# Performance work log

Measured on AMD Instinct MI355X. Metric: run time of the kernel, lower is better.

The kernel has to match this reference:

```python
import jax, jax.numpy as jnp
import numpy as np

N_NODES = 50000
N_EDGES = 800000
D_IN = 128
D_OUT = 128
N_GRAPHS = 512
N_CONVS = 5
EPS = 1e-5


def setup_inputs() -> dict:
    key = jax.random.key(0)
    ks = jax.random.split(key, 8)
    x = jax.random.normal(ks[0], (N_NODES, D_IN), dtype=jnp.float32)
    edge_index = jax.random.randint(ks[1], (2, N_EDGES), 0, N_NODES, dtype=jnp.int32)
    batch = jnp.sort(jax.random.randint(ks[2], (N_NODES,), 0, N_GRAPHS, dtype=jnp.int32))
    s = 1.0 / np.sqrt(D_IN)
    W_rel = jax.random.normal(ks[3], (N_CONVS, D_OUT, D_IN), dtype=jnp.float32) * s
    b_rel = jax.random.normal(ks[4], (N_CONVS, D_OUT), dtype=jnp.float32) * s
    W_root = jax.random.normal(ks[5], (N_CONVS, D_OUT, D_IN), dtype=jnp.float32) * s
    gamma = jnp.ones((D_OUT,), dtype=jnp.float32)
    beta = jnp.zeros((D_OUT,), dtype=jnp.float32)
    Wc = jax.random.normal(ks[6], (96, D_OUT), dtype=jnp.float32) * (1.0 / np.sqrt(D_OUT))
    bc = jax.random.normal(ks[7], (96,), dtype=jnp.float32) * (1.0 / np.sqrt(D_OUT))
    return {"x": x, "edge_index": edge_index, "batch": batch, "i": 0,
            "W_rel": W_rel, "b_rel": b_rel, "W_root": W_root,
            "gamma": gamma, "beta": beta, "Wc": Wc, "bc": bc}


def reference(x, edge_index, batch, i, W_rel, b_rel, W_root, gamma, beta, Wc, bc):
    # --- 5 GraphConv branches, summed. GraphConv: lin_rel(sum_{j->i} x_j) + lin_root(x).
    # Sum over the 5 convs commutes with the linears, so fold the weights first.
    src, dst = edge_index[0], edge_index[1]
    agg = jax.ops.segment_sum(x[src], dst, num_segments=N_NODES)  # [N, D_in]
    Wr = jnp.sum(W_rel, axis=0)   # [D_out, D_in]
    Wt = jnp.sum(W_root, axis=0)  # [D_out, D_in]
    br = jnp.sum(b_rel, axis=0)   # [D_out]
    h = agg @ Wr.T + x @ Wt.T + br  # [N, D_out]
    # --- NodeLevelBatchNorm (training: batch stats over all nodes, biased var)
    mean = jnp.mean(h, axis=0)
    var = jnp.mean((h - mean) ** 2, axis=0)
    h = gamma * (h - mean) * jax.lax.rsqrt(var + EPS) + beta
    # --- global max pool over graphs, relu, classifier (i=0 -> no-dropout branch)
    pooled = jax.ops.segment_max(h, batch, num_segments=N_GRAPHS)  # [G, D_out]
    pooled = jax.nn.relu(pooled)
    return pooled @ Wc.T + bc  # [G, 96]
```

## Files before the change

kernel.cpp:

```cpp
#include <hip/hip_runtime.h>

#define EPS 1e-5f

constexpr int NN = 50000, NE = 800000, DD = 128, NG = 512, NC = 5, NO = 96;
constexpr int MAXB = 8192;
constexpr int NBUCK = 196;

typedef __attribute__((ext_vector_type(8))) short bf16x8;
typedef __attribute__((ext_vector_type(4))) float f32x4;

constexpr size_t HB   = 0;
constexpr size_t XB   = (size_t)NN * DD / 2;
constexpr size_t WB   = XB + (size_t)NN * DD / 2;
constexpr size_t BRO  = WB + DD * 256 / 2;
constexpr size_t CSUM = BRO + DD;
constexpr size_t CSQ  = CSUM + 4 * DD;
constexpr size_t POOL = CSQ + 4 * DD;
constexpr size_t ZLEN = 8 * DD + (size_t)NG * DD;
constexpr size_t GCNT = POOL + (size_t)NG * DD;
constexpr size_t ROFF = GCNT + 256;
constexpr size_t BSTOR= ROFF + NN + 1;
constexpr size_t CSR16= BSTOR + (size_t)NBUCK*MAXB;

constexpr int XCAST_B = NN * DD / 4 / 256;
constexpr int FOLD_B  = DD * DD / 256;
constexpr int BUCK_B  = (NE + 4095) / 4096;

static __device__ __forceinline__ unsigned short f2b(float f) {
    unsigned int u = __float_as_uint(f);
    return (unsigned short)((u + 0x7FFFu + ((u >> 16) & 1u)) >> 16);
}
static __device__ __forceinline__ float b2f(unsigned short h) {
    return __uint_as_float(((unsigned int)h) << 16);
}
static __device__ __forceinline__ unsigned fkey(float f) {
    unsigned u = __float_as_uint(f);
    return (u >> 31) ? ~u : (u | 0x80000000u);
}
static __device__ __forceinline__ float unfkey(unsigned k) {
    unsigned u = (k & 0x80000000u) ? (k ^ 0x80000000u) : ~k;
    return __uint_as_float(u);
}

__global__ __launch_bounds__(256) void k_prep(const float* __restrict__ x,
                                              const float* __restrict__ Wrel,
                                              const float* __restrict__ brel,
                                              const float* __restrict__ Wroot,
                                              const int* __restrict__ ei,
                                              float* __restrict__ ws, int* __restrict__ wi) {
    __shared__ int lcnt[256];
    __shared__ int lbase[256];
    int b = blockIdx.x, t = threadIdx.x;
    if (b < XCAST_B) {
        int i = b * 256 + t;
        float4 v = ((const float4*)x)[i];
        ushort4 o = {f2b(v.x), f2b(v.y), f2b(v.z), f2b(v.w)};
        ((ushort4*)(ws + XB))[i] = o;
    } else if (b < XCAST_B + FOLD_B) {
        int idx = (b - XCAST_B) * 256 + t;
        int k = idx >> 7, o = idx & 127;
        float wr = 0.f, wt = 0.f;
        for (int c = 0; c < NC; ++c) {
            wr += Wrel [c*DD*DD + o*DD + k];
            wt += Wroot[c*DD*DD + o*DD + k];
        }
        unsigned short* wb = (unsigned short*)(ws + WB);
        wb[o*256 + k]       = f2b(wr);
        wb[o*256 + 128 + k] = f2b(wt);
        if (k == 0) {
            float bias = 0.f;
            for (int c = 0; c < NC; ++c) bias += brel[c*DD + o];
            ws[BRO + o] = bias;
        }
    } else {
        int bb = b - XCAST_B - FOLD_B;
        lcnt[t] = 0;
        __syncthreads();
        int val[16], krk[16];
        #pragma unroll
        for (int j = 0; j < 16; ++j) {
            int e = bb * 4096 + j * 256 + t;
            krk[j] = -1;
            if (e < NE) {
                int d = ei[NE + e], s = ei[e];
                int key = d >> 8;
                int r = atomicAdd(&lcnt[key], 1);
                val[j] = s | ((d & 255) << 16);
                krk[j] = (key << 16) | r;
            }
        }
        __syncthreads();
        if (t < NBUCK && lcnt[t] > 0)
            lbase[t] = atomicAdd(&wi[GCNT + t], lcnt[t]);
        __syncthreads();
        #pragma unroll
        for (int j = 0; j < 16; ++j) {
            if (krk[j] >= 0) {
                int key = krk[j] >> 16, r = krk[j] & 0xFFFF;
                int p = lbase[key] + r;
                if (p < MAXB) wi[BSTOR + (size_t)key * MAXB + p] = val[j];
            }
        }
    }
}

__global__ __launch_bounds__(256) void k_sort(int* __restrict__ wi) {
    __shared__ int eds[MAXB];
    __shared__ unsigned short srt[MAXB];
    __shared__ int cnt[256], cnt2[256], lscan[256], gall[256];
    int t = threadIdx.x, b = blockIdx.x;
    for (size_t i = (size_t)b * 256 + t; i < ZLEN; i += (size_t)NBUCK * 256)
        wi[CSUM + i] = 0;
    int g = wi[GCNT + t];
    gall[t] = g; lscan[t] = g; cnt[t] = 0;
    __syncthreads();
    for (int off = 1; off < 256; off <<= 1) {
        int u = (t >= off) ? gall[t - off] : 0;
        __syncthreads();
        gall[t] += u;
        __syncthreads();
    }
    int base = gall[b] - lscan[b];
    int C = lscan[b]; if (C > MAXB) C = MAXB;
    __syncthreads();
    for (int i = t; i < C; i += 256) {
        int v = wi[BSTOR + (size_t)b * MAXB + i];
        eds[i] = v;
        atomicAdd(&cnt[v >> 16], 1);
    }
    __syncthreads();
    int cv = cnt[t];
    for (int off = 1; off < 256; off <<= 1) {
        int u = (t >= off) ? cnt[t - off] : 0;
        __syncthreads();
        cnt[t] += u;
        __syncthreads();
    }
    lscan[t] = cnt[t] - cv;
    cnt2[t] = 0;
    __syncthreads();
    int n = b * 256 + t;
    if (n < NN) wi[ROFF + n] = base + lscan[t];
    if (b == 0 && t == 0) wi[ROFF + NN] = NE;
    for (int i = t; i < C; i += 256) {
        int v = eds[i], k = v >> 16;
        int p = lscan[k] + atomicAdd(&cnt2[k], 1);
        srt[p] = (unsigned short)(v & 0xFFFF);
    }
    __syncthreads();
    unsigned short* csr = (unsigned short*)(wi + CSR16);
    for (int i = t; i < C; i += 256)
        csr[base + i] = srt[i];
}

__global__ __launch_bounds__(256) void k_gather(const int* __restrict__ wi,
                                                float* __restrict__ ws) {
    const unsigned short* xb = (const unsigned short*)(ws + XB);
    const unsigned short* csr = (const unsigned short*)(wi + CSR16);
    unsigned short* hb = (unsigned short*)(ws + HB);
    int tid = threadIdx.x;
    int n   = blockIdx.x * 16 + (tid >> 4);
    int sub = tid & 15;
    int c8  = sub * 8;
    if (n >= NN) return;
    int e0 = wi[ROFF + n], e1 = wi[ROFF + n + 1];
    int cnt = e1 - e0;
    float acc0[8] = {}, acc1[8] = {};
    int base = 0;
    for (; base + 16 <= cnt; base += 16) {
        int myE = (int)csr[e0 + base + sub];
        #pragma unroll
        for (int h = 0; h < 2; ++h) {
            bf16x8 v[8];
            #pragma unroll
            for (int j = 0; j < 8; ++j) {
                int s = __shfl(myE, h * 8 + j, 16);
                v[j] = *(const bf16x8*)&xb[(size_t)s * DD + c8];
            }
            #pragma unroll
            for (int j = 0; j < 8; ++j)
                #pragma unroll
                for (int c = 0; c < 8; ++c)
                    ((j & 1) ? acc1 : acc0)[c] += b2f((unsigned short)v[j][c]);
        }
    }
    int rem = cnt - base;
    if (rem > 0) {
        int myE = (sub < rem) ? (int)csr[e0 + base + sub] : 0;
        int j = 0;
        for (; j + 8 <= rem; j += 8) {
            bf16x8 v[8];
            #pragma unroll
            for (int q = 0; q < 8; ++q) {
                int s = __shfl(myE, j + q, 16);
                v[q] = *(const bf16x8*)&xb[(size_t)s * DD + c8];
            }
            #pragma unroll
            for (int q = 0; q < 8; ++q)
                #pragma unroll
                for (int c = 0; c < 8; ++c)
                    ((q & 1) ? acc1 : acc0)[c] += b2f((unsigned short)v[q][c]);
        }
        if (j + 4 <= rem) {
            bf16x8 v[4];
            #pragma unroll
            for (int q = 0; q < 4; ++q) {
                int s = __shfl(myE, j + q, 16);
                v[q] = *(const bf16x8*)&xb[(size_t)s * DD + c8];
            }
            #pragma unroll
            for (int q = 0; q < 4; ++q)
                #pragma unroll
                for (int c = 0; c < 8; ++c)
                    ((q & 1) ? acc1 : acc0)[c] += b2f((unsigned short)v[q][c]);
            j += 4;
        }
        for (; j < rem; ++j) {
            int s = __shfl(myE, j, 16);
            bf16x8 v = *(const bf16x8*)&xb[(size_t)s * DD + c8];
            #pragma unroll
            for (int c = 0; c < 8; ++c) acc0[c] += b2f((unsigned short)v[c]);
        }
    }
    bf16x8 o;
    #pragma unroll
    for (int c = 0; c < 8; ++c) o[c] = (short)f2b(acc0[c] + acc1[c]);
    *(bf16x8*)&hb[(size_t)n * DD + c8] = o;
}

__global__ __launch_bounds__(256) void k_gemm(const int* __restrict__ batch,
                                              float* __restrict__ ws) {
    __shared__ float sSum[128], sSq[128];
    __shared__ int batchS[64];
    __shared__ unsigned maxS[8][128];
    const unsigned short* hb = (const unsigned short*)(ws + HB);
    const unsigned short* xb = (const unsigned short*)(ws + XB);
    const unsigned short* wb = (const unsigned short*)(ws + WB);
    unsigned* poolU = (unsigned*)(ws + POOL);
    int tid  = threadIdx.x;
    if (tid < 128) { sSum[tid] = 0.f; sSq[tid] = 0.f; }
    for (int i = tid; i < 8 * 128; i += 256) ((unsigned*)maxS)[i] = 0u;
    if (tid < 64) {
        int r = blockIdx.x * 64 + tid; if (r > NN - 1) r = NN - 1;
        batchS[tid] = batch[r];
    }
    __syncthreads();
    int gBase = batchS[0];
    int wave = tid >> 6, lane = tid & 63;
    int quad = lane >> 4, l16 = lane & 15;
    int cw = wave * 32;
    bf16x8 bf[2][8];
    #pragma unroll
    for (int nt = 0; nt < 2; ++nt)
        #pragma unroll
        for (int kt = 0; kt < 8; ++kt)
            bf[nt][kt] = *(const bf16x8*)(wb + (size_t)(cw + nt*16 + l16)*256 + kt*32 + quad*8);
    float bias[2] = { ws[BRO + cw + l16], ws[BRO + cw + 16 + l16] };
    float csum[2] = {}, csq[2] = {};
    #pragma unroll
    for (int rt = 0; rt < 4; ++rt) {
        int lbase = rt * 16;
        int row0 = blockIdx.x * 64 + lbase;
        int arow = row0 + l16; if (arow > NN - 1) arow = NN - 1;
        const unsigned short* aggRow = hb + (size_t)arow * DD;
        const unsigned short* xRow   = xb + (size_t)arow * DD;
        bf16x8 af[8];
        #pragma unroll
        for (int kt = 0; kt < 8; ++kt)
            af[kt] = *(const bf16x8*)((kt < 4 ? aggRow + kt*32 : xRow + kt*32 - 128) + quad*8);
        f32x4 acc[2] = {};
        #pragma unroll
        for (int kt = 0; kt < 8; ++kt)
            #pragma unroll
            for (int nt = 0; nt < 2; ++nt)
                acc[nt] = __builtin_amdgcn_mfma_f32_16x16x32_bf16(af[kt], bf[nt][kt], acc[nt], 0, 0, 0);
        #pragma unroll
        for (int nt = 0; nt < 2; ++nt) {
            int col = cw + nt*16 + l16;
            float mx = 0.f; int gcur = -1;
            #pragma unroll
            for (int r = 0; r < 4; ++r) {
                int row = row0 + quad*4 + r;
                if (row < NN) {
                    float v = acc[nt][r] + bias[nt];
                    csum[nt] += v; csq[nt] += v * v;
                    int g = batchS[lbase + quad*4 + r];
                    if (g != gcur) {
                        if (gcur >= 0) {
                            int rel = gcur - gBase;
                            if (rel < 8) atomicMax(&maxS[rel][col], fkey(mx));
                            else atomicMax(&poolU[(size_t)gcur * DD + col], fkey(mx));
                        }
                        gcur = g; mx = v;
                    } else mx = fmaxf(mx, v);
                }
            }
            if (gcur >= 0) {
                int rel = gcur - gBase;
                if (rel < 8) atomicMax(&maxS[rel][col], fkey(mx));
                else atomicMax(&poolU[(size_t)gcur * DD + col], fkey(mx));
            }
        }
    }
    __syncthreads();
    int span = batchS[63] - gBase + 1; if (span > 8) span = 8;
    for (int i = tid; i < span * 128; i += 256) {
        unsigned k = maxS[i >> 7][i & 127];
        if (k) atomicMax(&poolU[(size_t)(gBase + (i >> 7)) * DD + (i & 127)], k);
    }
    #pragma unroll
    for (int nt = 0; nt < 2; ++nt) {
        int col = cw + nt*16 + l16;
        float cs = csum[nt], cq = csq[nt];
        cs += __shfl_xor(cs, 16); cs += __shfl_xor(cs, 32);
        cq += __shfl_xor(cq, 16); cq += __shfl_xor(cq, 32);
        if (quad == 0) { atomicAdd(&sSum[col], cs); atomicAdd(&sSq[col], cq); }
    }
    __syncthreads();
    if (tid < 128) {
        int slot = (blockIdx.x & 3) * DD;
        atomicAdd(&ws[CSUM + slot + tid], sSum[tid]);
        atomicAdd(&ws[CSQ  + slot + tid], sSq[tid]);
    }
}

__global__ __launch_bounds__(128) void k_out(const float* __restrict__ gamma,
                                             const float* __restrict__ beta,
                                             const float* __restrict__ Wc,
                                             const float* __restrict__ bc,
                                             const float* __restrict__ ws,
                                             float* __restrict__ out) {
    __shared__ float pS[128];
    int g = blockIdx.x, t = threadIdx.x;
    float s = ws[CSUM + t] + ws[CSUM + DD + t] + ws[CSUM + 2*DD + t] + ws[CSUM + 3*DD + t];
    float q = ws[CSQ  + t] + ws[CSQ  + DD + t] + ws[CSQ  + 2*DD + t] + ws[CSQ  + 3*DD + t];
    float mean = s * (1.0f / NN);
    float var  = q * (1.0f / NN) - mean * mean;
    float sc   = gamma[t] * rsqrtf(var + EPS);
    float sh   = beta[t] - sc * mean;
    unsigned k = ((const unsigned*)(ws + POOL))[(size_t)g * DD + t];
    float p = 0.f;
    if (k) p = fmaxf(unfkey(k) * sc + sh, 0.f);
    pS[t] = p;
    __syncthreads();
    if (t < NO) {
        float acc = bc[t];
        #pragma unroll 8
        for (int kk = 0; kk < DD; ++kk) acc += pS[kk] * Wc[t*DD + kk];
        out[g*NO + t] = acc;
    }
}

extern "C" void kernel_launch(void* const* d_in, const int* in_sizes, int n_in,
                              void* d_out, int out_size, void* d_ws, size_t ws_size,
                              hipStream_t stream) {
    const float* x     = (const float*)d_in[0];
    const int*   ei    = (const int*)  d_in[1];
    const int*   batch = (const int*)  d_in[2];
    const float* Wrel  = (const float*)d_in[4];
    const float* brel  = (const float*)d_in[5];
    const float* Wroot = (const float*)d_in[6];
    const float* gamma = (const float*)d_in[7];
    const float* beta  = (const float*)d_in[8];
    const float* Wc    = (const float*)d_in[9];
    const float* bc    = (const float*)d_in[10];
    float* ws  = (float*)d_ws;
    int*   wi  = (int*)d_ws;
    float* out = (float*)d_out;

    hipMemsetAsync(wi + GCNT, 0, 256 * sizeof(int), stream);

    k_prep  <<<XCAST_B + FOLD_B + BUCK_B, 256, 0, stream>>>(x, Wrel, brel, Wroot, ei, ws, wi);
    k_sort  <<<NBUCK, 256, 0, stream>>>(wi);
    k_gather<<<(NN + 15)/16, 256, 0, stream>>>(wi, ws);
    k_gemm  <<<(NN + 63)/64, 256, 0, stream>>>(batch, ws);
    k_out   <<<NG, 128, 0, stream>>>(gamma, beta, Wc, bc, ws, out);
}
```

Baseline: 183.5 us.

## Fuse all stages into one persistent kernel with software grid barriers

Replaces the five separate kernel launches with a single persistent kernel of 512 blocks. The blocks loop over virtual block indices for each phase (prep, bucket sort, gather, GEMM+pool, output) and separate the phases with atomic-counter grid barriers. The memset of the bucket counters moves into the kernel's zeroing phase. This removes per-launch overhead and tail gaps between kernels. In exchange it relies on all 512 blocks being co-resident to avoid deadlock, adds spin-wait barrier cost, and limits parallelism per phase to the fixed grid size.

```diff
diff --git a/kernel.cpp b/kernel.cpp
--- a/kernel.cpp
+++ b/kernel.cpp
@@ -5,6 +5,7 @@
 constexpr int NN = 50000, NE = 800000, DD = 128, NG = 512, NC = 5, NO = 96;
 constexpr int MAXB = 8192;
 constexpr int NBUCK = 196;
+constexpr int GRIDB = 512;
 
 typedef __attribute__((ext_vector_type(8))) short bf16x8;
 typedef __attribute__((ext_vector_type(4))) float f32x4;
@@ -16,15 +17,19 @@
 constexpr size_t CSUM = BRO + DD;
 constexpr size_t CSQ  = CSUM + 4 * DD;
 constexpr size_t POOL = CSQ + 4 * DD;
-constexpr size_t ZLEN = 8 * DD + (size_t)NG * DD;
 constexpr size_t GCNT = POOL + (size_t)NG * DD;
-constexpr size_t ROFF = GCNT + 256;
+constexpr size_t ZLEN = 8 * DD + (size_t)NG * DD + 256;
+constexpr size_t BAR  = GCNT + 256;
+constexpr size_t ROFF = BAR + 8;
 constexpr size_t BSTOR= ROFF + NN + 1;
 constexpr size_t CSR16= BSTOR + (size_t)NBUCK*MAXB;
 
 constexpr int XCAST_B = NN * DD / 4 / 256;
 constexpr int FOLD_B  = DD * DD / 256;
 constexpr int BUCK_B  = (NE + 4095) / 4096;
+constexpr int PREP_V  = XCAST_B + FOLD_B + BUCK_B;
+constexpr int GATH_V  = (NN + 15) / 16;
+constexpr int GEMM_V  = (NN + 63) / 64;
 
 static __device__ __forceinline__ unsigned short f2b(float f) {
     unsigned int u = __float_as_uint(f);
@@ -42,312 +47,353 @@
     return __uint_as_float(u);
 }
 
-__global__ __launch_bounds__(256) void k_prep(const float* __restrict__ x,
-                                              const float* __restrict__ Wrel,
-                                              const float* __restrict__ brel,
-                                              const float* __restrict__ Wroot,
-                                              const int* __restrict__ ei,
-                                              float* __restrict__ ws, int* __restrict__ wi) {
-    __shared__ int lcnt[256];
-    __shared__ int lbase[256];
-    int b = blockIdx.x, t = threadIdx.x;
-    if (b < XCAST_B) {
-        int i = b * 256 + t;
-        float4 v = ((const float4*)x)[i];
-        ushort4 o = {f2b(v.x), f2b(v.y), f2b(v.z), f2b(v.w)};
-        ((ushort4*)(ws + XB))[i] = o;
-    } else if (b < XCAST_B + FOLD_B) {
-        int idx = (b - XCAST_B) * 256 + t;
-        int k = idx >> 7, o = idx & 127;
-        float wr = 0.f, wt = 0.f;
-        for (int c = 0; c < NC; ++c) {
-            wr += Wrel [c*DD*DD + o*DD + k];
-            wt += Wroot[c*DD*DD + o*DD + k];
+static __device__ __forceinline__ void gridbar(int* bar, int idx, int nb) {
+    __syncthreads();
+    if (threadIdx.x == 0) {
+        __threadfence();
+        atomicAdd(&bar[idx], 1);
+        while (atomicAdd(&bar[idx], 0) < nb)
+            __builtin_amdgcn_s_sleep(8);
+        __threadfence();
+    }
+    __syncthreads();
+}
+
+__global__ __launch_bounds__(256, 2) void k_mega(const float* __restrict__ x,
+                                                 const float* __restrict__ Wrel,
+                                                 const float* __restrict__ brel,
+                                                 const float* __restrict__ Wroot,
+                                                 const int* __restrict__ ei,
+                                                 const int* __restrict__ batch,
+                                                 const float* __restrict__ gamma,
+                                                 const float* __restrict__ beta,
+                                                 const float* __restrict__ Wc,
+                                                 const float* __restrict__ bc,
+                                                 float* __restrict__ ws,
+                                                 int* __restrict__ wi,
+                                                 float* __restrict__ out) {
+    __shared__ __align__(16) char smem[53248];
+    const int t   = threadIdx.x;
+    const int bid = blockIdx.x;
+    const int nb  = gridDim.x;
+    int* bar = wi + BAR;
+
+    for (size_t i = (size_t)bid * 256 + t; i < ZLEN; i += (size_t)nb * 256)
+        wi[CSUM + i] = 0;
+    gridbar(bar, 0, nb);
+
+    {
+        int* lcnt  = (int*)(smem + 49152);
+        int* lbase = (int*)(smem + 50176);
+        for (int vb = bid; vb < PREP_V; vb += nb) {
+            if (vb < XCAST_B) {
+                int i = vb * 256 + t;
+                float4 v = ((const float4*)x)[i];
+                ushort4 o = {f2b(v.x), f2b(v.y), f2b(v.z), f2b(v.w)};
+                ((ushort4*)(ws + XB))[i] = o;
+            } else if (vb < XCAST_B + FOLD_B) {
+                int idx = (vb - XCAST_B) * 256 + t;
+                int k = idx >> 7, o = idx & 127;
+                float wr = 0.f, wt = 0.f;
+                for (int c = 0; c < NC; ++c) {
+                    wr += Wrel [c*DD*DD + o*DD + k];
+                    wt += Wroot[c*DD*DD + o*DD + k];
+                }
+                unsigned short* wb = (unsigned short*)(ws + WB);
+                wb[o*256 + k]       = f2b(wr);
+                wb[o*256 + 128 + k] = f2b(wt);
+                if (k == 0) {
+                    float bias = 0.f;
+                    for (int c = 0; c < NC; ++c) bias += brel[c*DD + o];
+                    ws[BRO + o] = bias;
+                }
+            } else {
+                int bb = vb - XCAST_B - FOLD_B;
+                lcnt[t] = 0;
+                __syncthreads();
+                int val[16], krk[16];
+                #pragma unroll
+                for (int j = 0; j < 16; ++j) {
+                    int e = bb * 4096 + j * 256 + t;
+                    krk[j] = -1;
+                    if (e < NE) {
+                        int d = ei[NE + e], s = ei[e];
+                        int key = d >> 8;
+                        int r = atomicAdd(&lcnt[key], 1);
+                        val[j] = s | ((d & 255) << 16);
+                        krk[j] = (key << 16) | r;
+                    }
+                }
+                __syncthreads();
+                if (t < NBUCK && lcnt[t] > 0)
+                    lbase[t] = atomicAdd(&wi[GCNT + t], lcnt[t]);
+                __syncthreads();
+                #pragma unroll
+                for (int j = 0; j < 16; ++j) {
+                    if (krk[j] >= 0) {
+                        int key = krk[j] >> 16, r = krk[j] & 0xFFFF;
+                        int p = lbase[key] + r;
+                        if (p < MAXB) wi[BSTOR + (size_t)key * MAXB + p] = val[j];
+                    }
+                }
+                __syncthreads();
+            }
         }
-        unsigned short* wb = (unsigned short*)(ws + WB);
-        wb[o*256 + k]       = f2b(wr);
-        wb[o*256 + 128 + k] = f2b(wt);
-        if (k == 0) {
-            float bias = 0.f;
-            for (int c = 0; c < NC; ++c) bias += brel[c*DD + o];
-            ws[BRO + o] = bias;
+    }
+    gridbar(bar, 1, nb);
+
+    {
+        int* eds   = (int*)smem;
+        unsigned short* srt = (unsigned short*)(smem + 32768);
+        int* cnt   = (int*)(smem + 49152);
+        int* cnt2  = (int*)(smem + 50176);
+        int* lscan = (int*)(smem + 51200);
+        int* gall  = (int*)(smem + 52224);
+        for (int b = bid; b < NBUCK; b += nb) {
+            int g = wi[GCNT + t];
+            gall[t] = g; lscan[t] = g; cnt[t] = 0;
+            __syncthreads();
+            for (int off = 1; off < 256; off <<= 1) {
+                int u = (t >= off) ? gall[t - off] : 0;
+                __syncthreads();
+                gall[t] += u;
+                __syncthreads();
+            }
+            int base = gall[b] - lscan[b];
+            int C = lscan[b]; if (C > MAXB) C = MAXB;
+            __syncthreads();
+            for (int i = t; i < C; i += 256) {
+                int v = wi[BSTOR + (size_t)b * MAXB + i];
+                eds[i] = v;
+                atomicAdd(&cnt[v >> 16], 1);
+            }
+            __syncthreads();
+            int cv = cnt[t];
+            for (int off = 1; off < 256; off <<= 1) {
+                int u = (t >= off) ? cnt[t - off] : 0;
+                __syncthreads();
+                cnt[t] += u;
+                __syncthreads();
+            }
+            lscan[t] = cnt[t] - cv;
+            cnt2[t] = 0;
+            __syncthreads();
+            int n = b * 256 + t;
+            if (n < NN) wi[ROFF + n] = base + lscan[t];
+            if (b == 0 && t == 0) wi[ROFF + NN] = NE;
+            for (int i = t; i < C; i += 256) {
+                int v = eds[i], k = v >> 16;
+                int p = lscan[k] + atomicAdd(&cnt2[k], 1);
+                srt[p] = (unsigned short)(v & 0xFFFF);
+            }
+            __syncthreads();
+            unsigned short* csr = (unsigned short*)(wi + CSR16);
+            for (int i = t; i < C; i += 256)
+                csr[base + i] = srt[i];
         }
-    } else {
-        int bb = b - XCAST_B - FOLD_B;
-        lcnt[t] = 0;
-        __syncthreads();
-        int val[16], krk[16];
-        #pragma unroll
-        for (int j = 0; j < 16; ++j) {
-            int e = bb * 4096 + j * 256 + t;
-            krk[j] = -1;
-            if (e < NE) {
-                int d = ei[NE + e], s = ei[e];
-                int key = d >> 8;
-                int r = atomicAdd(&lcnt[key], 1);
-                val[j] = s | ((d & 255) << 16);
-                krk[j] = (key << 16) | r;
+    }
+    gridbar(bar, 2, nb);
+
+    {
+        const unsigned short* xb  = (const unsigned short*)(ws + XB);
+        const unsigned short* csr = (const unsigned short*)(wi + CSR16);
+        unsigned short* hb = (unsigned short*)(ws + HB);
+        int sub = t & 15;
+        int c8  = sub * 8;
+        for (int vb = bid; vb < GATH_V; vb += nb) {
+            int n = vb * 16 + (t >> 4);
+            if (n < NN) {
+                int e0 = wi[ROFF + n], e1 = wi[ROFF + n + 1];
+                int cnt = e1 - e0;
+                float acc0[8] = {}, acc1[8] = {};
+                int base = 0;
+                for (; base + 16 <= cnt; base += 16) {
+                    int myE = (int)csr[e0 + base + sub];
+                    #pragma unroll
+                    for (int h = 0; h < 2; ++h) {
+                        bf16x8 v[8];
+                        #pragma unroll
+                        for (int j = 0; j < 8; ++j) {
+                            int s = __shfl(myE, h * 8 + j, 16);
+                            v[j] = *(const bf16x8*)&xb[(size_t)s * DD + c8];
+                        }
+                        #pragma unroll
+                        for (int j = 0; j < 8; ++j)
+                            #pragma unroll
+                            for (int c = 0; c < 8; ++c)
+                                ((j & 1) ? acc1 : acc0)[c] += b2f((unsigned short)v[j][c]);
+                    }
+                }
+                int rem = cnt - base;
+                if (rem > 0) {
+                    int myE = (sub < rem) ? (int)csr[e0 + base + sub] : 0;
+                    int j = 0;
+                    for (; j + 8 <= rem; j += 8) {
+                        bf16x8 v[8];
+                        #pragma unroll
+                        for (int q = 0; q < 8; ++q) {
+                            int s = __shfl(myE, j + q, 16);
+                            v[q] = *(const bf16x8*)&xb[(size_t)s * DD + c8];
+                        }
+                        #pragma unroll
+                        for (int q = 0; q < 8; ++q)
+                            #pragma unroll
+                            for (int c = 0; c < 8; ++c)
+                                ((q & 1) ? acc1 : acc0)[c] += b2f((unsigned short)v[q][c]);
+                    }
+                    if (j + 4 <= rem) {
+                        bf16x8 v[4];
+                        #pragma unroll
+                        for (int q = 0; q < 4; ++q) {
+                            int s = __shfl(myE, j + q, 16);
+                            v[q] = *(const bf16x8*)&xb[(size_t)s * DD + c8];
+                        }
+                        #pragma unroll
+                        for (int q = 0; q < 4; ++q)
+                            #pragma unroll
+                            for (int c = 0; c < 8; ++c)
+                                ((q & 1) ? acc1 : acc0)[c] += b2f((unsigned short)v[q][c]);
+                        j += 4;
+                    }
+                    for (; j < rem; ++j) {
+                        int s = __shfl(myE, j, 16);
+                        bf16x8 v = *(const bf16x8*)&xb[(size_t)s * DD + c8];
+                        #pragma unroll
+                        for (int c = 0; c < 8; ++c) acc0[c] += b2f((unsigned short)v[c]);
+                    }
+                }
+                bf16x8 o;
+                #pragma unroll
+                for (int c = 0; c < 8; ++c) o[c] = (short)f2b(acc0[c] + acc1[c]);
+                *(bf16x8*)&hb[(size_t)n * DD + c8] = o;
             }
         }
-        __syncthreads();
-        if (t < NBUCK && lcnt[t] > 0)
-            lbase[t] = atomicAdd(&wi[GCNT + t], lcnt[t]);
-        __syncthreads();
-        #pragma unroll
-        for (int j = 0; j < 16; ++j) {
-            if (krk[j] >= 0) {
-                int key = krk[j] >> 16, r = krk[j] & 0xFFFF;
-                int p = lbase[key] + r;
-                if (p < MAXB) wi[BSTOR + (size_t)key * MAXB + p] = val[j];
-            }
-        }
-    }
-}
-
-__global__ __launch_bounds__(256) void k_sort(int* __restrict__ wi) {
-    __shared__ int eds[MAXB];
-    __shared__ unsigned short srt[MAXB];
-    __shared__ int cnt[256], cnt2[256], lscan[256], gall[256];
-    int t = threadIdx.x, b = blockIdx.x;
-    for (size_t i = (size_t)b * 256 + t; i < ZLEN; i += (size_t)NBUCK * 256)
-        wi[CSUM + i] = 0;
-    int g = wi[GCNT + t];
-    gall[t] = g; lscan[t] = g; cnt[t] = 0;
-    __syncthreads();
-    for (int off = 1; off < 256; off <<= 1) {
-        int u = (t >= off) ? gall[t - off] : 0;
-        __syncthreads();
-        gall[t] += u;
-        __syncthreads();
-    }
-    int base = gall[b] - lscan[b];
-    int C = lscan[b]; if (C > MAXB) C = MAXB;
-    __syncthreads();
-    for (int i = t; i < C; i += 256) {
-        int v = wi[BSTOR + (size_t)b * MAXB + i];
-        eds[i] = v;
-        atomicAdd(&cnt[v >> 16], 1);
-    }
-    __syncthreads();
-    int cv = cnt[t];
-    for (int off = 1; off < 256; off <<= 1) {
-        int u = (t >= off) ? cnt[t - off] : 0;
-        __syncthreads();
-        cnt[t] += u;
-        __syncthreads();
-    }
-    lscan[t] = cnt[t] - cv;
-    cnt2[t] = 0;
-    __syncthreads();
-    int n = b * 256 + t;
-    if (n < NN) wi[ROFF + n] = base + lscan[t];
-    if (b == 0 && t == 0) wi[ROFF + NN] = NE;
-    for (int i = t; i < C; i += 256) {
-        int v = eds[i], k = v >> 16;
-        int p = lscan[k] + atomicAdd(&cnt2[k], 1);
-        srt[p] = (unsigned short)(v & 0xFFFF);
-    }
-    __syncthreads();
-    unsigned short* csr = (unsigned short*)(wi + CSR16);
-    for (int i = t; i < C; i += 256)
-        csr[base + i] = srt[i];
-}
-
-__global__ __launch_bounds__(256) void k_gather(const int* __restrict__ wi,
-                                                float* __restrict__ ws) {
-    const unsigned short* xb = (const unsigned short*)(ws + XB);
-    const unsigned short* csr = (const unsigned short*)(wi + CSR16);
-    unsigned short* hb = (unsigned short*)(ws + HB);
-    int tid = threadIdx.x;
-    int n   = blockIdx.x * 16 + (tid >> 4);
-    int sub = tid & 15;
-    int c8  = sub * 8;
-    if (n >= NN) return;
-    int e0 = wi[ROFF + n], e1 = wi[ROFF + n + 1];
-    int cnt = e1 - e0;
-    float acc0[8] = {}, acc1[8] = {};
-    int base = 0;
-    for (; base + 16 <= cnt; base += 16) {
-        int myE = (int)csr[e0 + base + sub];
-        #pragma unroll
-        for (int h = 0; h < 2; ++h) {
-            bf16x8 v[8];
-            #pragma unroll
-            for (int j = 0; j < 8; ++j) {
-                int s = __shfl(myE, h * 8 + j, 16);
-                v[j] = *(const bf16x8*)&xb[(size_t)s * DD + c8];
-            }
-            #pragma unroll
-            for (int j = 0; j < 8; ++j)
-                #pragma unroll
-                for (int c = 0; c < 8; ++c)
-                    ((j & 1) ? acc1 : acc0)[c] += b2f((unsigned short)v[j][c]);
-        }
-    }
-    int rem = cnt - base;
-    if (rem > 0) {
-        int myE = (sub < rem) ? (int)csr[e0 + base + sub] : 0;
-        int j = 0;
-        for (; j + 8 <= rem; j += 8) {
-            bf16x8 v[8];
-            #pragma unroll
-            for (int q = 0; q < 8; ++q) {
-                int s = __shfl(myE, j + q, 16);
-                v[q] = *(const bf16x8*)&xb[(size_t)s * DD + c8];
-            }
-            #pragma unroll
-            for (int q = 0; q < 8; ++q)
-                #pragma unroll
-                for (int c = 0; c < 8; ++c)
-                    ((q & 1) ? acc1 : acc0)[c] += b2f((unsigned short)v[q][c]);
-        }
-        if (j + 4 <= rem) {
-            bf16x8 v[4];
-            #pragma unroll
-            for (int q = 0; q < 4; ++q) {
-                int s = __shfl(myE, j + q, 16);
-                v[q] = *(const bf16x8*)&xb[(size_t)s * DD + c8];
-            }
-            #pragma unroll
-            for (int q = 0; q < 4; ++q)
-                #pragma unroll
-                for (int c = 0; c < 8; ++c)
-                    ((q & 1) ? acc1 : acc0)[c] += b2f((unsigned short)v[q][c]);
-            j += 4;
-        }
-        for (; j < rem; ++j) {
-            int s = __shfl(myE, j, 16);
-            bf16x8 v = *(const bf16x8*)&xb[(size_t)s * DD + c8];
-            #pragma unroll
-            for (int c = 0; c < 8; ++c) acc0[c] += b2f((unsigned short)v[c]);
-        }
-    }
-    bf16x8 o;
-    #pragma unroll
-    for (int c = 0; c < 8; ++c) o[c] = (short)f2b(acc0[c] + acc1[c]);
-    *(bf16x8*)&hb[(size_t)n * DD + c8] = o;
-}
-
-__global__ __launch_bounds__(256) void k_gemm(const int* __restrict__ batch,
-                                              float* __restrict__ ws) {
-    __shared__ float sSum[128], sSq[128];
-    __shared__ int batchS[64];
-    __shared__ unsigned maxS[8][128];
-    const unsigned short* hb = (const unsigned short*)(ws + HB);
-    const unsigned short* xb = (const unsigned short*)(ws + XB);
-    const unsigned short* wb = (const unsigned short*)(ws + WB);
-    unsigned* poolU = (unsigned*)(ws + POOL);
-    int tid  = threadIdx.x;
-    if (tid < 128) { sSum[tid] = 0.f; sSq[tid] = 0.f; }
-    for (int i = tid; i < 8 * 128; i += 256) ((unsigned*)maxS)[i] = 0u;
-    if (tid < 64) {
-        int r = blockIdx.x * 64 + tid; if (r > NN - 1) r = NN - 1;
-        batchS[tid] = batch[r];
-    }
-    __syncthreads();
-    int gBase = batchS[0];
-    int wave = tid >> 6, lane = tid & 63;
-    int quad = lane >> 4, l16 = lane & 15;
-    int cw = wave * 32;
-    bf16x8 bf[2][8];
-    #pragma unroll
-    for (int nt = 0; nt < 2; ++nt)
-        #pragma unroll
-        for (int kt = 0; kt < 8; ++kt)
-            bf[nt][kt] = *(const bf16x8*)(wb + (size_t)(cw + nt*16 + l16)*256 + kt*32 + quad*8);
-    float bias[2] = { ws[BRO + cw + l16], ws[BRO + cw + 16 + l16] };
-    float csum[2] = {}, csq[2] = {};
-    #pragma unroll
-    for (int rt = 0; rt < 4; ++rt) {
-        int lbase = rt * 16;
-        int row0 = blockIdx.x * 64 + lbase;
-        int arow = row0 + l16; if (arow > NN - 1) arow = NN - 1;
-        const unsigned short* aggRow = hb + (size_t)arow * DD;
-        const unsigned short* xRow   = xb + (size_t)arow * DD;
-        bf16x8 af[8];
-        #pragma unroll
-        for (int kt = 0; kt < 8; ++kt)
-            af[kt] = *(const bf16x8*)((kt < 4 ? aggRow + kt*32 : xRow + kt*32 - 128) + quad*8);
-        f32x4 acc[2] = {};
-        #pragma unroll
-        for (int kt = 0; kt < 8; ++kt)
+    }
+    gridbar(bar, 3, nb);
+
+    {
+        float* sSum = (float*)smem;
+        float* sSq  = (float*)(smem + 512);
+        int*   batchS = (int*)(smem + 1024);
+        unsigned (*maxS)[128] = (unsigned(*)[128])(smem + 1536);
+        const unsigned short* hb = (const unsigned short*)(ws + HB);
+        const unsigned short* xb = (const unsigned short*)(ws + XB);
+        const unsigned short* wb = (const unsigned short*)(ws + WB);
+        unsigned* poolU = (unsigned*)(ws + POOL);
+        int wave = t >> 6, lane = t & 63;
+        int quad = lane >> 4, l16 = lane & 15;
+        int cw = wave * 32;
+        for (int vb = bid; vb < GEMM_V; vb += nb) {
+            if (t < 128) { sSum[t] = 0.f; sSq[t] = 0.f; }
+            for (int i = t; i < 8 * 128; i += 256) ((unsigned*)maxS)[i] = 0u;
+            if (t < 64) {
+                int r = vb * 64 + t; if (r > NN - 1) r = NN - 1;
+                batchS[t] = batch[r];
+            }
+            __syncthreads();
+            int gBase = batchS[0];
+            bf16x8 bf[2][8];
             #pragma unroll
             for (int nt = 0; nt < 2; ++nt)
-                acc[nt] = __builtin_amdgcn_mfma_f32_16x16x32_bf16(af[kt], bf[nt][kt], acc[nt], 0, 0, 0);
-        #pragma unroll
-        for (int nt = 0; nt < 2; ++nt) {
-            int col = cw + nt*16 + l16;
-            float mx = 0.f; int gcur = -1;
+                #pragma unroll
+                for (int kt = 0; kt < 8; ++kt)
+                    bf[nt][kt] = *(const bf16x8*)(wb + (size_t)(cw + nt*16 + l16)*256 + kt*32 + quad*8);
+            float bias[2] = { ws[BRO + cw + l16], ws[BRO + cw + 16 + l16] };
+            float csum[2] = {}, csq[2] = {};
             #pragma unroll
-            for (int r = 0; r < 4; ++r) {
-                int row = row0 + quad*4 + r;
-                if (row < NN) {
-                    float v = acc[nt][r] + bias[nt];
-                    csum[nt] += v; csq[nt] += v * v;
-                    int g = batchS[lbase + quad*4 + r];
-                    if (g != gcur) {
-                        if (gcur >= 0) {
-                            int rel = gcur - gBase;
-                            if (rel < 8) atomicMax(&maxS[rel][col], fkey(mx));
-                            else atomicMax(&poolU[(size_t)gcur * DD + col], fkey(mx));
+            for (int rt = 0; rt < 4; ++rt) {
+                int lbase = rt * 16;
+                int row0 = vb * 64 + lbase;
+                int arow = row0 + l16; if (arow > NN - 1) arow = NN - 1;
+                const unsigned short* aggRow = hb + (size_t)arow * DD;
+                const unsigned short* xRow   = xb + (size_t)arow * DD;
+                bf16x8 af[8];
+                #pragma unroll
+                for (int kt = 0; kt < 8; ++kt)
+                    af[kt] = *(const bf16x8*)((kt < 4 ? aggRow + kt*32 : xRow + kt*32 - 128) + quad*8);
+                f32x4 acc[2] = {};
+                #pragma unroll
+                for (int kt = 0; kt < 8; ++kt)
+                    #pragma unroll
+                    for (int nt = 0; nt < 2; ++nt)
+                        acc[nt] = __builtin_amdgcn_mfma_f32_16x16x32_bf16(af[kt], bf[nt][kt], acc[nt], 0, 0, 0);
+                #pragma unroll
+                for (int nt = 0; nt < 2; ++nt) {
+                    int col = cw + nt*16 + l16;
+                    float mx = 0.f; int gcur = -1;
+                    #pragma unroll
+                    for (int r = 0; r < 4; ++r) {
+                        int row = row0 + quad*4 + r;
+                        if (row < NN) {
+                            float v = acc[nt][r] + bias[nt];
+                            csum[nt] += v; csq[nt] += v * v;
+                            int g = batchS[lbase + quad*4 + r];
+                            if (g != gcur) {
+                                if (gcur >= 0) {
+                                    int rel = gcur - gBase;
+                                    if (rel < 8) atomicMax(&maxS[rel][col], fkey(mx));
+                                    else atomicMax(&poolU[(size_t)gcur * DD + col], fkey(mx));
+                                }
+                                gcur = g; mx = v;
+                            } else mx = fmaxf(mx, v);
                         }
-                        gcur = g; mx = v;
-                    } else mx = fmaxf(mx, v);
-                }
-            }
-            if (gcur >= 0) {
-                int rel = gcur - gBase;
-                if (rel < 8) atomicMax(&maxS[rel][col], fkey(mx));
-                else atomicMax(&poolU[(size_t)gcur * DD + col], fkey(mx));
-            }
+                    }
+                    if (gcur >= 0) {
+                        int rel = gcur - gBase;
+                        if (rel < 8) atomicMax(&maxS[rel][col], fkey(mx));
+                        else atomicMax(&poolU[(size_t)gcur * DD + col], fkey(mx));
+                    }
+                }
+            }
+            __syncthreads();
+            int span = batchS[63] - gBase + 1; if (span > 8) span = 8;
+            for (int i = t; i < span * 128; i += 256) {
+                unsigned k = maxS[i >> 7][i & 127];
+                if (k) atomicMax(&poolU[(size_t)(gBase + (i >> 7)) * DD + (i & 127)], k);
+            }
+            #pragma unroll
+            for (int nt = 0; nt < 2; ++nt) {
+                int col = cw + nt*16 + l16;
+                float cs = csum[nt], cq = csq[nt];
+                cs += __shfl_xor(cs, 16); cs += __shfl_xor(cs, 32);
+                cq += __shfl_xor(cq, 16); cq += __shfl_xor(cq, 32);
+                if (quad == 0) { atomicAdd(&sSum[col], cs); atomicAdd(&sSq[col], cq); }
+            }
+            __syncthreads();
+            if (t < 128) {
+                int slot = (vb & 3) * DD;
+                atomicAdd(&ws[CSUM + slot + t], sSum[t]);
+                atomicAdd(&ws[CSQ  + slot + t], sSq[t]);
+            }
+            __syncthreads();
         }
     }
-    __syncthreads();
-    int span = batchS[63] - gBase + 1; if (span > 8) span = 8;
-    for (int i = tid; i < span * 128; i += 256) {
-        unsigned k = maxS[i >> 7][i & 127];
-        if (k) atomicMax(&poolU[(size_t)(gBase + (i >> 7)) * DD + (i & 127)], k);
-    }
-    #pragma unroll
-    for (int nt = 0; nt < 2; ++nt) {
-        int col = cw + nt*16 + l16;
-        float cs = csum[nt], cq = csq[nt];
-        cs += __shfl_xor(cs, 16); cs += __shfl_xor(cs, 32);
-        cq += __shfl_xor(cq, 16); cq += __shfl_xor(cq, 32);
-        if (quad == 0) { atomicAdd(&sSum[col], cs); atomicAdd(&sSq[col], cq); }
-    }
-    __syncthreads();
-    if (tid < 128) {
-        int slot = (blockIdx.x & 3) * DD;
-        atomicAdd(&ws[CSUM + slot + tid], sSum[tid]);
-        atomicAdd(&ws[CSQ  + slot + tid], sSq[tid]);
-    }
-}
-
-__global__ __launch_bounds__(128) void k_out(const float* __restrict__ gamma,
-                                             const float* __restrict__ beta,
-                                             const float* __restrict__ Wc,
-                                             const float* __restrict__ bc,
-                                             const float* __restrict__ ws,
-                                             float* __restrict__ out) {
-    __shared__ float pS[128];
-    int g = blockIdx.x, t = threadIdx.x;
-    float s = ws[CSUM + t] + ws[CSUM + DD + t] + ws[CSUM + 2*DD + t] + ws[CSUM + 3*DD + t];
-    float q = ws[CSQ  + t] + ws[CSQ  + DD + t] + ws[CSQ  + 2*DD + t] + ws[CSQ  + 3*DD + t];
-    float mean = s * (1.0f / NN);
-    float var  = q * (1.0f / NN) - mean * mean;
-    float sc   = gamma[t] * rsqrtf(var + EPS);
-    float sh   = beta[t] - sc * mean;
-    unsigned k = ((const unsigned*)(ws + POOL))[(size_t)g * DD + t];
-    float p = 0.f;
-    if (k) p = fmaxf(unfkey(k) * sc + sh, 0.f);
-    pS[t] = p;
-    __syncthreads();
-    if (t < NO) {
-        float acc = bc[t];
-        #pragma unroll 8
-        for (int kk = 0; kk < DD; ++kk) acc += pS[kk] * Wc[t*DD + kk];
-        out[g*NO + t] = acc;
+    gridbar(bar, 4, nb);
+
+    {
+        float* pS = (float*)smem;
+        int half = t >> 7, tt = t & 127;
+        for (int vb = bid; vb < NG / 2; vb += nb) {
+            int g = vb * 2 + half;
+            float s = ws[CSUM + tt] + ws[CSUM + DD + tt] + ws[CSUM + 2*DD + tt] + ws[CSUM + 3*DD + tt];
+            float q = ws[CSQ  + tt] + ws[CSQ  + DD + tt] + ws[CSQ  + 2*DD + tt] + ws[CSQ  + 3*DD + tt];
+            float mean = s * (1.0f / NN);
+            float var  = q * (1.0f / NN) - mean * mean;
+            float sc   = gamma[tt] * rsqrtf(var + EPS);
+            float sh   = beta[tt] - sc * mean;
+            unsigned k = ((const unsigned*)(ws + POOL))[(size_t)g * DD + tt];
+            float p = 0.f;
+            if (k) p = fmaxf(unfkey(k) * sc + sh, 0.f);
+            pS[half * 128 + tt] = p;
+            __syncthreads();
+            if (tt < NO) {
+                float acc = bc[tt];
+                #pragma unroll 8
+                for (int kk = 0; kk < DD; ++kk) acc += pS[half * 128 + kk] * Wc[tt*DD + kk];
+                out[g*NO + tt] = acc;
+            }
+            __syncthreads();
+        }
     }
 }
 
@@ -368,11 +414,8 @@
     int*   wi  = (int*)d_ws;
     float* out = (float*)d_out;
 
-    hipMemsetAsync(wi + GCNT, 0, 256 * sizeof(int), stream);
-
-    k_prep  <<<XCAST_B + FOLD_B + BUCK_B, 256, 0, stream>>>(x, Wrel, brel, Wroot, ei, ws, wi);
-    k_sort  <<<NBUCK, 256, 0, stream>>>(wi);
-    k_gather<<<(NN + 15)/16, 256, 0, stream>>>(wi, ws);
-    k_gemm  <<<(NN + 63)/64, 256, 0, stream>>>(batch, ws);
-    k_out   <<<NG, 128, 0, stream>>>(gamma, beta, Wc, bc, ws, out);
-}
+    hipMemsetAsync(wi + BAR, 0, 8 * sizeof(int), stream);
+
+    hipLaunchKernelGGL(k_mega, dim3(GRIDB), dim3(256), 0, stream,
+                       x, Wrel, brel, Wroot, ei, batch, gamma, beta, Wc, bc, ws, wi, out);
+}
```

New measurement: 413.8 us. +125.5%, slower.
